# Kernel optimization log

Hardware: AMD Instinct MI355X
Metric: run time of the kernel (lower is better)

The kernel has to match this reference:

```python
import jax, jax.numpy as jnp
import numpy as np

N = 65536   # batch
G = 7       # grid
C = 2       # classes (cats vs dogs)
A = 3       # anchors


def _bce(p, t):
    return -(t * jnp.log(p) + (1.0 - t) * jnp.log(1.0 - p))


def _iou(a, b):
    # a, b: [..., 4] boxes in (cx, cy, w, h) format
    ax1, ay1 = a[..., 0] - a[..., 2] / 2, a[..., 1] - a[..., 3] / 2
    ax2, ay2 = a[..., 0] + a[..., 2] / 2, a[..., 1] + a[..., 3] / 2
    bx1, by1 = b[..., 0] - b[..., 2] / 2, b[..., 1] - b[..., 3] / 2
    bx2, by2 = b[..., 0] + b[..., 2] / 2, b[..., 1] + b[..., 3] / 2
    iw = jnp.clip(jnp.minimum(ax2, bx2) - jnp.maximum(ax1, bx1), 0.0)
    ih = jnp.clip(jnp.minimum(ay2, by2) - jnp.maximum(ay1, by1), 0.0)
    inter = iw * ih
    union = (ax2 - ax1) * (ay2 - ay1) + (bx2 - bx1) * (by2 - by1) - inter
    return inter / (union + 1e-9)


def setup_inputs():
    key = jax.random.key(0)
    k1, k2, k3, k4 = jax.random.split(key, 4)
    # probabilities / box params must lie strictly in (0,1) for BCE and log()
    bbox_ = jax.random.uniform(k1, (N, 15, G, G), dtype=jnp.float32, minval=0.01, maxval=0.99)
    bbox = jax.random.uniform(k2, (N, 5, G, G), dtype=jnp.float32, minval=0.01, maxval=0.99)
    cls_ = jax.random.normal(k3, (N, C), dtype=jnp.float32)
    cls = jax.random.randint(k4, (N,), 1, 3).astype(jnp.int64)  # labels in {1,2}
    return {"bbox_": bbox_, "cls_": cls_, "bbox": bbox, "cls": cls}


def reference(bbox_, cls_, bbox, cls):
    n = bbox.shape[0]
    bidx = jnp.arange(n)

    # classification: CrossEntropyLoss (mean) with labels cls-1
    logp = jax.nn.log_softmax(cls_, axis=-1)
    ce = -jnp.mean(jnp.take_along_axis(logp, (cls - 1)[:, None], axis=1))

    # argmax cell of GT objectness map per sample
    probs = bbox[:, 0]                       # [N,7,7]
    m = jnp.argmax(probs.reshape(n, -1), axis=1)
    i, j = m // G, m % G                     # [N], [N]

    cell_gt = bbox[bidx, :, i, j]            # [N,5]
    cell_pr = bbox_[bidx, :, i, j].reshape(n, A, 5)  # [N,3,5]

    jf = j.astype(bbox.dtype)
    if_ = i.astype(bbox.dtype)

    # target box in global coords
    tgt = jnp.stack([(cell_gt[:, 1] + jf) / G, (cell_gt[:, 2] + if_) / G,
                     cell_gt[:, 3], cell_gt[:, 4]], axis=-1)          # [N,4]
    # anchor boxes in global coords
    anc = jnp.stack([(cell_pr[:, :, 1] + jf[:, None]) / G,
                     (cell_pr[:, :, 2] + if_[:, None]) / G,
                     cell_pr[:, :, 3], cell_pr[:, :, 4]], axis=-1)    # [N,3,4]

    best = jnp.argmax(_iou(anc, tgt[:, None, :]), axis=1)             # [N]

    # target objectness maps: best anchor channel gets GT prob map
    target_prob = jnp.zeros((n, A, G, G), dtype=bbox.dtype)
    target_prob = target_prob.at[bidx, best].set(probs)

    # coordinate BCE (sum) + size L1-of-logs (sum) at the matched cell/anchor
    best_box = cell_pr[bidx, best]           # [N,5]
    coord = jnp.sum(_bce(best_box[:, 1:3], cell_gt[:, 1:3]))
    size = jnp.sum(jnp.abs(jnp.log(best_box[:, 3:5]) - jnp.log(cell_gt[:, 3:5])))

    # per-anchor objectness BCE (mean over N*49 each)
    prob_loss = (jnp.mean(_bce(bbox_[:, 0], target_prob[:, 0]))
                 + jnp.mean(_bce(bbox_[:, 5], target_prob[:, 1]))
                 + jnp.mean(_bce(bbox_[:, 10], target_prob[:, 2])))

    return ce + coord + size + prob_loss
```

## Files before the change

kernel.cpp:

```cpp
#include <hip/hip_runtime.h>
#include <math.h>


static constexpr int GG_ = 49;

__global__ void zero_kernel(float* out) { if (threadIdx.x == 0) out[0] = 0.0f; }

__global__ __launch_bounds__(256) void loss_kernel(
    const float* __restrict__ pr_all,
    const float* __restrict__ cls_logits,
    const float* __restrict__ gt_all,
    const int*   __restrict__ cls_lbl,
    float* __restrict__ out, int N)
{
    const int lane   = threadIdx.x & 63;
    const int wid    = blockIdx.x * (blockDim.x >> 6) + (threadIdx.x >> 6);
    const int nwaves = gridDim.x * (blockDim.x >> 6);
    const float invG   = 1.0f / 7.0f;
    const float invN   = 1.0f / (float)N;
    const float invN49 = 1.0f / ((float)N * 49.0f);

    float acc = 0.0f;

    for (int n = wid; n < N; n += nwaves) {
        const float* gt = gt_all + (size_t)n * (5  * GG_);
        const float* pr = pr_all + (size_t)n * (15 * GG_);

        float t = -1.0f;
        if (lane < GG_) t = gt[lane];

        float v = t; int idx = lane;
        #pragma unroll
        for (int off = 32; off; off >>= 1) {
            float v2 = __shfl_xor(v, off);
            int   i2 = __shfl_xor(idx, off);
            if (v2 > v || (v2 == v && i2 < idx)) { v = v2; idx = i2; }
        }
        const int m  = idx;
        const int mi = m / 7, mj = m - mi * 7;
        const float jf = (float)mj, if_ = (float)mi;

        float p0 = 0.5f, p1 = 0.5f, p2 = 0.5f;
        if (lane < GG_) {
            p0 = pr[lane];
            p1 = pr[5  * GG_ + lane];
            p2 = pr[10 * GG_ + lane];
        }

        float cellv = 0.0f;
        if (lane >= 1 && lane <= 4) {
            cellv = gt[lane * GG_ + m];
        } else if (lane >= 5 && lane < 17) {
            int k = lane - 5;
            int a = k >> 2, c = k & 3;
            cellv = pr[(5 * a + 1 + c) * GG_ + m];
        }

        const float g1 = __shfl(cellv, 1);
        const float g2 = __shfl(cellv, 2);
        const float g3 = __shfl(cellv, 3);
        const float g4 = __shfl(cellv, 4);

        const float tx  = (g1 + jf) * invG;
        const float ty  = (g2 + if_) * invG;
        const float tx1 = tx - g3 * 0.5f, tx2 = tx + g3 * 0.5f;
        const float ty1 = ty - g4 * 0.5f, ty2 = ty + g4 * 0.5f;
        const float tarea = (tx2 - tx1) * (ty2 - ty1);

        int best = 0; float bestIoU = -1.0f;
        #pragma unroll
        for (int a = 0; a < 3; a++) {
            float c1 = __shfl(cellv, 5 + 4 * a + 0);
            float c2 = __shfl(cellv, 5 + 4 * a + 1);
            float c3 = __shfl(cellv, 5 + 4 * a + 2);
            float c4 = __shfl(cellv, 5 + 4 * a + 3);
            float ax  = (c1 + jf) * invG;
            float ay  = (c2 + if_) * invG;
            float ax1 = ax - c3 * 0.5f, ax2 = ax + c3 * 0.5f;
            float ay1 = ay - c4 * 0.5f, ay2 = ay + c4 * 0.5f;
            float iw = fminf(ax2, tx2) - fmaxf(ax1, tx1); iw = fmaxf(iw, 0.0f);
            float ih = fminf(ay2, ty2) - fmaxf(ay1, ty1); ih = fmaxf(ih, 0.0f);
            float inter = iw * ih;
            float uni   = (ax2 - ax1) * (ay2 - ay1) + tarea - inter;
            float iou   = inter / (uni + 1e-9f);
            if (iou > bestIoU) { bestIoU = iou; best = a; }
        }

        const float px = __shfl(cellv, 5 + 4 * best + 0);
        const float py = __shfl(cellv, 5 + 4 * best + 1);
        const float pw = __shfl(cellv, 5 + 4 * best + 2);
        const float ph = __shfl(cellv, 5 + 4 * best + 3);

        float s = 0.0f;
        if (lane < GG_) {
            float l1p0 = __logf(1.0f - p0);
            float l1p1 = __logf(1.0f - p1);
            float l1p2 = __logf(1.0f - p2);
            s = -(l1p0 + l1p1 + l1p2);
            float pb   = (best == 0) ? p0 : ((best == 1) ? p1 : p2);
            float l1pb = (best == 0) ? l1p0 : ((best == 1) ? l1p1 : l1p2);
            s -= t * (__logf(pb) - l1pb);
        }
        acc += s * invN49;

        if (lane == 0) {
            float coord = -(g1 * __logf(px) + (1.0f - g1) * __logf(1.0f - px))
                          -(g2 * __logf(py) + (1.0f - g2) * __logf(1.0f - py));
            float size  = fabsf(__logf(pw) - __logf(g3))
                        + fabsf(__logf(ph) - __logf(g4));
            float x0 = cls_logits[2 * n], x1 = cls_logits[2 * n + 1];
            int   c  = cls_lbl[n] - 1;
            float mx  = fmaxf(x0, x1);
            float lse = mx + __logf(__expf(x0 - mx) + __expf(x1 - mx));
            float lp  = ((c == 0) ? x0 : x1) - lse;
            acc += coord + size - lp * invN;
        }
    }

    #pragma unroll
    for (int off = 32; off; off >>= 1) acc += __shfl_xor(acc, off);
    __shared__ float wsum[4];
    if (lane == 0) wsum[threadIdx.x >> 6] = acc;
    __syncthreads();
    if (threadIdx.x == 0) {
        atomicAdd(out, wsum[0] + wsum[1] + wsum[2] + wsum[3]);
    }
}

extern "C" void kernel_launch(void* const* d_in, const int* in_sizes, int n_in,
                              void* d_out, int out_size, void* d_ws, size_t ws_size,
                              hipStream_t stream) {
    const float* bbox_p = (const float*)d_in[0];
    const float* cls_p  = (const float*)d_in[1];
    const float* bbox_g = (const float*)d_in[2];
    const int*   cls_l  = (const int*)d_in[3];
    float* out = (float*)d_out;
    const int N = in_sizes[3];

    hipLaunchKernelGGL(zero_kernel, dim3(1), dim3(64), 0, stream, out);
    hipLaunchKernelGGL(loss_kernel, dim3(2048), dim3(256), 0, stream,
                       bbox_p, cls_p, bbox_g, cls_l, out, N);
}
```

Measured before the change: 309.0 us.

## Stage full per-sample prediction and GT tensors in LDS via coalesced loads

Each wave now issues all its global loads for a sample up front: the full 735-float prediction block, the 245-float GT block, the class logits and the label, read contiguously and clamped at the end. It writes them to a per-wave LDS slab, then serves the dependent argmax-cell gathers and best-anchor lookups from LDS instead of issuing a second round of scattered global loads. This is meant to remove the serialized global-memory round trip that followed the argmax. The cost is reading every channel of the sample instead of only the needed ones, plus extra register and LDS pressure. The objectness log terms are remapped onto the loaded register layout by lane ranges.

```diff
diff --git a/kernel.cpp b/kernel.cpp
--- a/kernel.cpp
+++ b/kernel.cpp
@@ -3,6 +3,8 @@
 
 
 static constexpr int GG_ = 49;
+static constexpr int PRD = 15 * GG_;
+static constexpr int GTD = 5  * GG_;
 
 __global__ void zero_kernel(float* out) { if (threadIdx.x == 0) out[0] = 0.0f; }
 
@@ -14,21 +16,49 @@
     float* __restrict__ out, int N)
 {
     const int lane   = threadIdx.x & 63;
-    const int wid    = blockIdx.x * (blockDim.x >> 6) + (threadIdx.x >> 6);
+    const int wslot  = threadIdx.x >> 6;
+    const int wid    = blockIdx.x * (blockDim.x >> 6) + wslot;
     const int nwaves = gridDim.x * (blockDim.x >> 6);
     const float invG   = 1.0f / 7.0f;
     const float invN   = 1.0f / (float)N;
     const float invN49 = 1.0f / ((float)N * 49.0f);
 
+    __shared__ float lds_pr[4][768];
+    __shared__ float lds_gt[4][256];
+    float* __restrict__ Lpr = lds_pr[wslot];
+    float* __restrict__ Lgt = lds_gt[wslot];
+
     float acc = 0.0f;
 
     for (int n = wid; n < N; n += nwaves) {
-        const float* gt = gt_all + (size_t)n * (5  * GG_);
-        const float* pr = pr_all + (size_t)n * (15 * GG_);
+        const float* pr = pr_all + (size_t)n * PRD;
+        const float* gt = gt_all + (size_t)n * GTD;
 
-        float t = -1.0f;
-        if (lane < GG_) t = gt[lane];
+        float p[12];
+        #pragma unroll
+        for (int k = 0; k < 12; k++) {
+            int d = lane + 64 * k;
+            if (d > PRD - 1) d = PRD - 1;
+            p[k] = pr[d];
+        }
+        float g[4];
+        #pragma unroll
+        for (int k = 0; k < 4; k++) {
+            int d = lane + 64 * k;
+            if (d > GTD - 1) d = GTD - 1;
+            g[k] = gt[d];
+        }
+        const float x0 = cls_logits[2 * n];
+        const float x1 = cls_logits[2 * n + 1];
+        const int   c  = cls_lbl[n] - 1;
 
+        #pragma unroll
+        for (int k = 0; k < 12; k++) Lpr[lane + 64 * k] = p[k];
+        #pragma unroll
+        for (int k = 0; k < 4;  k++) Lgt[lane + 64 * k] = g[k];
+        asm volatile("s_waitcnt lgkmcnt(0)" ::: "memory");
+
+        const float t = (lane < GG_) ? g[0] : -1.0f;
         float v = t; int idx = lane;
         #pragma unroll
         for (int off = 32; off; off >>= 1) {
@@ -40,26 +70,10 @@
         const int mi = m / 7, mj = m - mi * 7;
         const float jf = (float)mj, if_ = (float)mi;
 
-        float p0 = 0.5f, p1 = 0.5f, p2 = 0.5f;
-        if (lane < GG_) {
-            p0 = pr[lane];
-            p1 = pr[5  * GG_ + lane];
-            p2 = pr[10 * GG_ + lane];
-        }
-
-        float cellv = 0.0f;
-        if (lane >= 1 && lane <= 4) {
-            cellv = gt[lane * GG_ + m];
-        } else if (lane >= 5 && lane < 17) {
-            int k = lane - 5;
-            int a = k >> 2, c = k & 3;
-            cellv = pr[(5 * a + 1 + c) * GG_ + m];
-        }
-
-        const float g1 = __shfl(cellv, 1);
-        const float g2 = __shfl(cellv, 2);
-        const float g3 = __shfl(cellv, 3);
-        const float g4 = __shfl(cellv, 4);
+        const float g1 = Lgt[ 49 + m];
+        const float g2 = Lgt[ 98 + m];
+        const float g3 = Lgt[147 + m];
+        const float g4 = Lgt[196 + m];
 
         const float tx  = (g1 + jf) * invG;
         const float ty  = (g2 + if_) * invG;
@@ -68,12 +82,13 @@
         const float tarea = (tx2 - tx1) * (ty2 - ty1);
 
         int best = 0; float bestIoU = -1.0f;
+        float px = 0.f, py = 0.f, pw = 0.f, ph = 0.f;
         #pragma unroll
         for (int a = 0; a < 3; a++) {
-            float c1 = __shfl(cellv, 5 + 4 * a + 0);
-            float c2 = __shfl(cellv, 5 + 4 * a + 1);
-            float c3 = __shfl(cellv, 5 + 4 * a + 2);
-            float c4 = __shfl(cellv, 5 + 4 * a + 3);
+            float c1 = Lpr[(5 * a + 1) * GG_ + m];
+            float c2 = Lpr[(5 * a + 2) * GG_ + m];
+            float c3 = Lpr[(5 * a + 3) * GG_ + m];
+            float c4 = Lpr[(5 * a + 4) * GG_ + m];
             float ax  = (c1 + jf) * invG;
             float ay  = (c2 + if_) * invG;
             float ax1 = ax - c3 * 0.5f, ax2 = ax + c3 * 0.5f;
@@ -83,23 +98,19 @@
             float inter = iw * ih;
             float uni   = (ax2 - ax1) * (ay2 - ay1) + tarea - inter;
             float iou   = inter / (uni + 1e-9f);
-            if (iou > bestIoU) { bestIoU = iou; best = a; }
+            if (iou > bestIoU) { bestIoU = iou; best = a; px = c1; py = c2; pw = c3; ph = c4; }
         }
 
-        const float px = __shfl(cellv, 5 + 4 * best + 0);
-        const float py = __shfl(cellv, 5 + 4 * best + 1);
-        const float pw = __shfl(cellv, 5 + 4 * best + 2);
-        const float ph = __shfl(cellv, 5 + 4 * best + 3);
+        float s = 0.0f;
+        if (lane < 49) s -= __logf(1.0f - p[0]);
+        if (lane >= 53) s -= __logf(1.0f - p[3]);
+        if (lane < 38) s -= __logf(1.0f - p[4]);
+        if (lane >= 42) s -= __logf(1.0f - p[7]);
+        if (lane < 27) s -= __logf(1.0f - p[8]);
 
-        float s = 0.0f;
         if (lane < GG_) {
-            float l1p0 = __logf(1.0f - p0);
-            float l1p1 = __logf(1.0f - p1);
-            float l1p2 = __logf(1.0f - p2);
-            s = -(l1p0 + l1p1 + l1p2);
-            float pb   = (best == 0) ? p0 : ((best == 1) ? p1 : p2);
-            float l1pb = (best == 0) ? l1p0 : ((best == 1) ? l1p1 : l1p2);
-            s -= t * (__logf(pb) - l1pb);
+            float pb = Lpr[245 * best + lane];
+            s -= t * (__logf(pb) - __logf(1.0f - pb));
         }
         acc += s * invN49;
 
@@ -108,8 +119,6 @@
                           -(g2 * __logf(py) + (1.0f - g2) * __logf(1.0f - py));
             float size  = fabsf(__logf(pw) - __logf(g3))
                         + fabsf(__logf(ph) - __logf(g4));
-            float x0 = cls_logits[2 * n], x1 = cls_logits[2 * n + 1];
-            int   c  = cls_lbl[n] - 1;
             float mx  = fmaxf(x0, x1);
             float lse = mx + __logf(__expf(x0 - mx) + __expf(x1 - mx));
             float lp  = ((c == 0) ? x0 : x1) - lse;
@@ -120,7 +129,7 @@
     #pragma unroll
     for (int off = 32; off; off >>= 1) acc += __shfl_xor(acc, off);
     __shared__ float wsum[4];
-    if (lane == 0) wsum[threadIdx.x >> 6] = acc;
+    if (lane == 0) wsum[wslot] = acc;
     __syncthreads();
     if (threadIdx.x == 0) {
         atomicAdd(out, wsum[0] + wsum[1] + wsum[2] + wsum[3]);
```

After: 314.5 us. Within noise of the previous version (+1.8%).
